# Performance work log

Measured on AMD Instinct MI355X. Metric: run time of the kernel, lower is better.

## Reference

```python
import jax, jax.numpy as jnp
import numpy as np

B, S, H = 4, 512, 256

def setup_inputs() -> dict:
    key = jax.random.key(0)
    k1, k2, k3, k4 = jax.random.split(key, 4)
    scale = 1.0 / np.sqrt(H)
    return {
        "h": jax.random.normal(k1, (B, S, H), dtype=jnp.float32),
        "W_t": jax.random.normal(k2, (H, H), dtype=jnp.float32) * scale,
        "W_t_prime": jax.random.normal(k3, (H, H), dtype=jnp.float32) * scale,
        "b_h": jnp.zeros((H,), dtype=jnp.float32),
        "W_a": jax.random.normal(k4, (H,), dtype=jnp.float32) * scale,
        "b_a": jnp.zeros((), dtype=jnp.float32),
    }

def reference(h, W_t, W_t_prime, b_h, W_a, b_a):
    # Project once per timestep, then broadcast-add over the (t, t') pair grid.
    ht = jnp.einsum("bsh,hk->bsk", h, W_t)          # W_t applied to h^t
    htp = jnp.einsum("bsh,hk->bsk", h, W_t_prime)   # W_{t'} applied to h^{t'}
    # transformed: (B, S_t, S_t', H)
    transformed = ht[:, :, None, :] + htp[:, None, :, :] + b_h
    tanh_out = jnp.tanh(transformed)
    scores = jnp.einsum("bsth,h->bst", tanh_out, W_a) + b_a  # (B, S, S)
    scores = jax.nn.sigmoid(scores)
    attention_weights = jax.nn.softmax(scores, axis=2)
    output = jnp.einsum("bst,bth->bsh", attention_weights, h)
    return output, attention_weights
```

## Files before the change

### kernel.cpp

```cpp
#include <hip/hip_runtime.h>

#define Bn 4
#define Sn 512
#define Hn 256

#define CC   2.8853900817779268f
#define L2E  1.4426950408889634f

typedef __attribute__((ext_vector_type(4))) float f32x4;
typedef __attribute__((ext_vector_type(2))) float f32x2;
typedef __attribute__((ext_vector_type(8))) short short8;

__device__ __forceinline__ unsigned short bf16rn(float f) {
    unsigned int u = __float_as_uint(f);
    u += 0x7fffu + ((u >> 16) & 1u);
    return (unsigned short)(u >> 16);
}
__device__ __forceinline__ float bf16tof(unsigned short b) {
    return __uint_as_float(((unsigned int)b) << 16);
}

__global__ __launch_bounds__(256) void prep_kernel(
    const float* __restrict__ h,  const float* __restrict__ Wt,
    const float* __restrict__ Wp, const float* __restrict__ Wa,
    const float* __restrict__ ba,
    unsigned short* __restrict__ h1, unsigned short* __restrict__ h2,
    unsigned short* __restrict__ wtp,
    float* __restrict__ wa2, float* __restrict__ cst)
{
    __shared__ float tile[64 * 68];
    __shared__ float red4[4];
    const int tid = threadIdx.x;
    const int bid = blockIdx.x;

    if (bid < 256) {
        const int base = (bid * 256 + tid) * 8;
        float4 v0 = *(const float4*)&h[base];
        float4 v1 = *(const float4*)&h[base + 4];
        float f[8] = {v0.x, v0.y, v0.z, v0.w, v1.x, v1.y, v1.z, v1.w};
        unsigned short b1[8], b2[8];
#pragma unroll
        for (int i = 0; i < 8; i++) {
            b1[i] = bf16rn(f[i]);
            b2[i] = bf16rn(f[i] - bf16tof(b1[i]));
        }
        uint4 u1, u2;
        u1.x = (unsigned)b1[0] | ((unsigned)b1[1] << 16);
        u1.y = (unsigned)b1[2] | ((unsigned)b1[3] << 16);
        u1.z = (unsigned)b1[4] | ((unsigned)b1[5] << 16);
        u1.w = (unsigned)b1[6] | ((unsigned)b1[7] << 16);
        u2.x = (unsigned)b2[0] | ((unsigned)b2[1] << 16);
        u2.y = (unsigned)b2[2] | ((unsigned)b2[3] << 16);
        u2.z = (unsigned)b2[4] | ((unsigned)b2[5] << 16);
        u2.w = (unsigned)b2[6] | ((unsigned)b2[7] << 16);
        *(uint4*)&h1[base] = u1;
        *(uint4*)&h2[base] = u2;

        if (bid == 0) {
            float w = Wa[tid];
#pragma unroll
            for (int off = 32; off >= 1; off >>= 1) w += __shfl_xor(w, off, 64);
            if ((tid & 63) == 0) red4[tid >> 6] = w;
            __syncthreads();
            wa2[tid] = -2.0f * Wa[tid];
            if (tid == 0)
                cst[0] = -L2E * ((red4[0] + red4[1] + red4[2] + red4[3]) + ba[0]);
        }
    } else {
        const int sb  = bid - 256;
        const int mat = sb >> 4;
        const int t4  = sb & 15;
        const int k0  = (t4 >> 2) * 64, n0 = (t4 & 3) * 64;
        const float* __restrict__ W = mat ? Wp : Wt;

#pragma unroll
        for (int i = 0; i < 4; i++) {
            const int idx = tid + 256 * i;
            const int kr = idx >> 4, nq = idx & 15;
            *(float4*)&tile[kr * 68 + nq * 4] =
                *(const float4*)&W[(k0 + kr) * Hn + n0 + nq * 4];
        }
        __syncthreads();

        unsigned short* p1 = wtp + mat * 2 * 65536;
        unsigned short* p2 = p1 + 65536;
#pragma unroll
        for (int i = 0; i < 8; i++) {
            const int idx = tid + 256 * i;
            const int n = idx >> 5, kp = idx & 31;
            const float f0 = tile[(2 * kp) * 68 + n];
            const float f1 = tile[(2 * kp + 1) * 68 + n];
            const unsigned short a0 = bf16rn(f0), a1 = bf16rn(f1);
            const unsigned short c0 = bf16rn(f0 - bf16tof(a0));
            const unsigned short c1 = bf16rn(f1 - bf16tof(a1));
            const int dw = ((n0 + n) * 256 + k0) / 2 + kp;
            ((unsigned int*)p1)[dw] = (unsigned)a0 | ((unsigned)a1 << 16);
            ((unsigned int*)p2)[dw] = (unsigned)c0 | ((unsigned)c1 << 16);
        }
    }
}

__global__ __launch_bounds__(256) void gemm_kernel(
    const unsigned short* __restrict__ h1, const unsigned short* __restrict__ h2,
    const unsigned short* __restrict__ wtp, const float* __restrict__ bh,
    float* __restrict__ Egt, float* __restrict__ Egp4)
{
    __shared__ char lds[20480];

    const int tid = threadIdx.x;
    const int mb = blockIdx.x >> 3;
    const int nb = blockIdx.x & 7;
    const int m0 = mb * 64;
    const bool isT = (nb < 4);
    const int n0l = isT ? nb * 64 : (nb - 4) * 64;
    const unsigned short* pB1 = wtp + (isT ? 0 : 2 * 65536);
    const unsigned short* pB2 = pB1 + 65536;

    const int w    = tid >> 6;
    const int lane = tid & 63;
    const int quad = lane >> 4;
    const int l15  = lane & 15;

    f32x4 acc[4];
#pragma unroll
    for (int i = 0; i < 4; i++) acc[i] = (f32x4){0.f, 0.f, 0.f, 0.f};

    const int ssel = tid >> 7;
    const int spl  = (tid >> 6) & 1;
    const int srow = (tid & 63) >> 2;
    const int sseg = tid & 3;
    const unsigned short* gsrc =
        (ssel == 0) ? (spl ? h2 : h1) : (spl ? pB2 : pB1);
    const int growbase = (ssel == 0) ? m0 : n0l;
    char* ldsdst = lds + (ssel * 2 + spl) * 5120;

    for (int ks = 0; ks < 256; ks += 32) {
        __syncthreads();
#pragma unroll
        for (int i = 0; i < 4; i++) {
            const int row = srow + i * 16;
            uint4 v = *(const uint4*)&gsrc[(growbase + row) * 256 + ks + sseg * 8];
            *(uint4*)(ldsdst + row * 80 + sseg * 16) = v;
        }
        __syncthreads();

        const char* Ab = lds;
        const char* Bb = lds + 10240;
        const short8 b1 = *(const short8*)(Bb + (w * 16 + l15) * 80 + quad * 16);
        const short8 b2 = *(const short8*)(Bb + 5120 + (w * 16 + l15) * 80 + quad * 16);
#pragma unroll
        for (int mt = 0; mt < 4; mt++) {
            const short8 a1 = *(const short8*)(Ab + (mt * 16 + l15) * 80 + quad * 16);
            const short8 a2 = *(const short8*)(Ab + 5120 + (mt * 16 + l15) * 80 + quad * 16);
            acc[mt] = __builtin_amdgcn_mfma_f32_16x16x32_bf16(a1, b1, acc[mt], 0, 0, 0);
            acc[mt] = __builtin_amdgcn_mfma_f32_16x16x32_bf16(a1, b2, acc[mt], 0, 0, 0);
            acc[mt] = __builtin_amdgcn_mfma_f32_16x16x32_bf16(a2, b1, acc[mt], 0, 0, 0);
        }
    }

    __syncthreads();
    float* ct = (float*)lds;
#pragma unroll
    for (int mt = 0; mt < 4; mt++)
#pragma unroll
        for (int r = 0; r < 4; r++)
            ct[(mt * 16 + quad * 4 + r) * 68 + w * 16 + l15] = acc[mt][r];
    __syncthreads();

    const int b  = m0 >> 9;
    const int s0 = m0 & 511;
    if (isT) {
        const int n0g = nb * 64;
#pragma unroll
        for (int i = 0; i < 4; i++) {
            const int item = tid + i * 256;
            const int mr = item >> 4, nq = item & 15;
            const float4 c  = *(const float4*)&ct[mr * 68 + nq * 4];
            const float4 bv = *(const float4*)&bh[n0g + nq * 4];
            float4 o;
            o.x = __builtin_amdgcn_exp2f((c.x + bv.x) * CC);
            o.y = __builtin_amdgcn_exp2f((c.y + bv.y) * CC);
            o.z = __builtin_amdgcn_exp2f((c.z + bv.z) * CC);
            o.w = __builtin_amdgcn_exp2f((c.w + bv.w) * CC);
            *(float4*)&Egt[(m0 + mr) * Hn + n0g + nq * 4] = o;
        }
    } else {
        const int kq0 = (nb - 4) * 16;
#pragma unroll
        for (int i = 0; i < 4; i++) {
            const int item = tid + i * 256;
            const int mr = item & 63, nq = item >> 6;
            const float4 c = *(const float4*)&ct[mr * 68 + nq * 4];
            float4 o;
            o.x = __builtin_amdgcn_exp2f(c.x * CC);
            o.y = __builtin_amdgcn_exp2f(c.y * CC);
            o.z = __builtin_amdgcn_exp2f(c.z * CC);
            o.w = __builtin_amdgcn_exp2f(c.w * CC);
            *(float4*)&Egp4[b * 131072 + (kq0 + nq) * 2048 + (s0 + mr) * 4] = o;
        }
    }
}

__global__ __launch_bounds__(512) void attn_kernel(
    const float* __restrict__ hsrc, const float* __restrict__ Egt,
    const float* __restrict__ Egp4, const float* __restrict__ wa2,
    const float* __restrict__ cst,
    float* __restrict__ out, float* __restrict__ out_attn)
{
    __shared__ char smem[26624];
    float*  egt4   = (float*)smem;
    float*  attn_l = (float*)smem;
    float*  wal    = (float*)(smem + 8192);
    float*  red    = (float*)(smem + 9472);
    float4* part   = (float4*)(smem + 10240);

    const int tid = threadIdx.x;
    const int b   = blockIdx.x & 3;
    const int t0  = (blockIdx.x >> 2) << 2;

    for (int i = tid; i < 4 * Hn; i += 512)
        egt4[i] = Egt[(b * Sn + t0) * Hn + i];
    if (tid < 256) wal[tid] = wa2[tid];
    __syncthreads();

    const float4* __restrict__ ep = (const float4*)(Egp4 + b * (Hn * Sn));

    f32x2 accA[4], accB[4];
#pragma unroll
    for (int r = 0; r < 4; r++) { accA[r] = (f32x2){0.f, 0.f}; accB[r] = (f32x2){0.f, 0.f}; }

    float4 cur = ep[tid];
    float4 nxt = ep[Sn + tid];
    for (int k4 = 0; k4 < 64; k4++) {
        const float4 nn = ep[((k4 + 2) & 63) * Sn + tid];
        const float4 w4 = *(const float4*)&wal[k4 * 4];
        const f32x2 wa01 = (f32x2){w4.x, w4.y};
        const f32x2 wa23 = (f32x2){w4.z, w4.w};
        const f32x2 ep01 = (f32x2){cur.x, cur.y};
        const f32x2 ep23 = (f32x2){cur.z, cur.w};
#pragma unroll
        for (int r = 0; r < 4; r++) {
            const float4 eg = *(const float4*)&egt4[r * Hn + k4 * 4];
            const f32x2 d01 = ep01 * (f32x2){eg.x, eg.y} + (f32x2){1.f, 1.f};
            const f32x2 d23 = ep23 * (f32x2){eg.z, eg.w} + (f32x2){1.f, 1.f};
            const float p01 = d01.x * d01.y;
            const float p23 = d23.x * d23.y;
            const float rr  = __builtin_amdgcn_rcpf(p01 * p23);
            const float q23 = p23 * rr;
            const float q01 = p01 * rr;
            const f32x2 m01 = wa01 * (f32x2){d01.y, d01.x};
            const f32x2 m23 = wa23 * (f32x2){d23.y, d23.x};
            accA[r] = accA[r] + m01 * (f32x2){q23, q23};
            accB[r] = accB[r] + m23 * (f32x2){q01, q01};
        }
        cur = nxt; nxt = nn;
    }

    const float k0 = cst[0];
    float ex[4];
#pragma unroll
    for (int r = 0; r < 4; r++) {
        const float a = (accA[r].x + accA[r].y) + (accB[r].x + accB[r].y);
        const float e1  = __builtin_amdgcn_exp2f(fmaf(-L2E, a, k0));
        const float sig = __builtin_amdgcn_rcpf(1.0f + e1);
        ex[r] = __builtin_amdgcn_exp2f(L2E * sig);
    }

    const int lane = tid & 63, wid = tid >> 6;
#pragma unroll
    for (int r = 0; r < 4; r++) {
        float v = ex[r];
#pragma unroll
        for (int off = 32; off >= 1; off >>= 1) v += __shfl_xor(v, off, 64);
        if (lane == 0) red[r * 8 + wid] = v;
    }
    __syncthreads();

#pragma unroll
    for (int r = 0; r < 4; r++) {
        float tot = 0.f;
#pragma unroll
        for (int i = 0; i < 8; i++) tot += red[r * 8 + i];
        const float a = ex[r] * __builtin_amdgcn_rcpf(tot);
        attn_l[r * Sn + tid] = a;
        out_attn[(b * Sn + t0 + r) * Sn + tid] = a;
    }
    __syncthreads();

    const int c4 = tid & 63;
    const int q  = __builtin_amdgcn_readfirstlane(tid >> 6);

    const float* __restrict__ hb = hsrc + (b * Sn + q * 64) * Hn + c4 * 4;

    float4 a[4];
#pragma unroll
    for (int r = 0; r < 4; r++) a[r] = (float4){0.f, 0.f, 0.f, 0.f};

#pragma unroll 2
    for (int j4 = 0; j4 < 16; j4++) {
        float4 wv[4];
#pragma unroll
        for (int r = 0; r < 4; r++)
            wv[r] = *(const float4*)&attn_l[r * Sn + q * 64 + j4 * 4];
#pragma unroll
        for (int i = 0; i < 4; i++) {
            const float4 hv = *(const float4*)&hb[(j4 * 4 + i) * Hn];
#pragma unroll
            for (int r = 0; r < 4; r++) {
                const float wr = ((const float*)&wv[r])[i];
                a[r].x = fmaf(wr, hv.x, a[r].x);
                a[r].y = fmaf(wr, hv.y, a[r].y);
                a[r].z = fmaf(wr, hv.z, a[r].z);
                a[r].w = fmaf(wr, hv.w, a[r].w);
            }
        }
    }
    __syncthreads();

    if (q < 4) {
#pragma unroll
        for (int r = 0; r < 4; r++) part[(q * 4 + r) * 64 + c4] = a[r];
    }
    __syncthreads();
    if (q >= 4) {
#pragma unroll
        for (int r = 0; r < 4; r++) {
            float4 p = part[((q - 4) * 4 + r) * 64 + c4];
            p.x += a[r].x; p.y += a[r].y; p.z += a[r].z; p.w += a[r].w;
            part[((q - 4) * 4 + r) * 64 + c4] = p;
        }
    }
    __syncthreads();

    const int col = tid & 255;
    const int rh  = tid >> 8;
    const float* pf = (const float*)part;
#pragma unroll
    for (int rr = 0; rr < 2; rr++) {
        const int r = rh * 2 + rr;
        float s = 0.f;
#pragma unroll
        for (int qq = 0; qq < 4; qq++)
            s += pf[((qq * 4 + r) * 64 + (col >> 2)) * 4 + (col & 3)];
        out[(b * Sn + t0 + r) * Hn + col] = s;
    }
}

extern "C" void kernel_launch(void* const* d_in, const int* in_sizes, int n_in,
                              void* d_out, int out_size, void* d_ws, size_t ws_size,
                              hipStream_t stream) {
    const float* h   = (const float*)d_in[0];
    const float* Wt  = (const float*)d_in[1];
    const float* Wtp = (const float*)d_in[2];
    const float* bh  = (const float*)d_in[3];
    const float* Wa  = (const float*)d_in[4];
    const float* ba  = (const float*)d_in[5];

    float* out      = (float*)d_out;
    float* out_attn = out + Bn * Sn * Hn;

    float* ws   = (float*)d_ws;
    float* Egt  = ws;
    float* Egp4 = ws + 524288;
    float* wa2  = ws + 1048576;
    float* cst  = ws + 1048832;
    unsigned short* h1  = (unsigned short*)(ws + 1048840);
    unsigned short* h2  = h1 + 2048 * 256;
    unsigned short* wtp = h2 + 2048 * 256;

    prep_kernel<<<dim3(288), dim3(256), 0, stream>>>(
        h, Wt, Wtp, Wa, ba, h1, h2, wtp, wa2, cst);
    gemm_kernel<<<dim3(256), dim3(256), 0, stream>>>(h1, h2, wtp, bh, Egt, Egp4);
    attn_kernel<<<dim3(Bn * (Sn / 4)), dim3(512), 0, stream>>>(
        h, Egt, Egp4, wa2, cst, out, out_attn);
}
```

Before: 124.2 us.

## Split attention hidden-dim reduction across two thread halves with 1024-thread blocks

The attention kernel now launches 1024 threads per block. Each half of the block covers half of the hidden dimension for the score reduction, and the partial sums are combined through shared memory. The per-term math is rewritten as scalar FMAs with one reciprocal per four elements, and the prefetch pipeline is replaced by a plain loop. The output GEMV is also spread over 16 waves instead of 8. This buys more parallelism per block and more latency hiding, at the cost of extra barriers, idle threads during softmax, and possible register pressure under 1024-thread launch bounds.

```diff
diff --git a/kernel.cpp b/kernel.cpp
--- a/kernel.cpp
+++ b/kernel.cpp
@@ -8,7 +8,6 @@
 #define L2E  1.4426950408889634f
 
 typedef __attribute__((ext_vector_type(4))) float f32x4;
-typedef __attribute__((ext_vector_type(2))) float f32x2;
 typedef __attribute__((ext_vector_type(8))) short short8;
 
 __device__ __forceinline__ unsigned short bf16rn(float f) {
@@ -201,146 +200,147 @@
     }
 }
 
-__global__ __launch_bounds__(512) void attn_kernel(
+__global__ __launch_bounds__(1024) void attn_kernel(
     const float* __restrict__ hsrc, const float* __restrict__ Egt,
     const float* __restrict__ Egp4, const float* __restrict__ wa2,
     const float* __restrict__ cst,
     float* __restrict__ out, float* __restrict__ out_attn)
 {
-    __shared__ char smem[26624];
-    float*  egt4   = (float*)smem;
+    __shared__ char smem[40960];
     float*  attn_l = (float*)smem;
-    float*  wal    = (float*)(smem + 8192);
-    float*  red    = (float*)(smem + 9472);
-    float4* part   = (float4*)(smem + 10240);
+    float*  egt4   = (float*)(smem + 8192);
+    float*  wal    = (float*)(smem + 12288);
+    float*  accl   = (float*)(smem + 13312);
+    float*  red    = (float*)(smem + 21504);
+    float4* part   = (float4*)(smem + 8192);
 
     const int tid = threadIdx.x;
+    const int tp  = tid & 511;
+    const int kh  = tid >> 9;
     const int b   = blockIdx.x & 3;
     const int t0  = (blockIdx.x >> 2) << 2;
 
-    for (int i = tid; i < 4 * Hn; i += 512)
-        egt4[i] = Egt[(b * Sn + t0) * Hn + i];
+    egt4[tid & 1023] = Egt[(b * Sn + t0) * Hn + (tid & 1023)];
     if (tid < 256) wal[tid] = wa2[tid];
     __syncthreads();
 
     const float4* __restrict__ ep = (const float4*)(Egp4 + b * (Hn * Sn));
-
-    f32x2 accA[4], accB[4];
-#pragma unroll
-    for (int r = 0; r < 4; r++) { accA[r] = (f32x2){0.f, 0.f}; accB[r] = (f32x2){0.f, 0.f}; }
-
-    float4 cur = ep[tid];
-    float4 nxt = ep[Sn + tid];
-    for (int k4 = 0; k4 < 64; k4++) {
-        const float4 nn = ep[((k4 + 2) & 63) * Sn + tid];
-        const float4 w4 = *(const float4*)&wal[k4 * 4];
-        const f32x2 wa01 = (f32x2){w4.x, w4.y};
-        const f32x2 wa23 = (f32x2){w4.z, w4.w};
-        const f32x2 ep01 = (f32x2){cur.x, cur.y};
-        const f32x2 ep23 = (f32x2){cur.z, cur.w};
+    const int kb = kh * 32;
+
+    float acc[4] = {0.f, 0.f, 0.f, 0.f};
+
+#pragma unroll 2
+    for (int kk = 0; kk < 32; kk++) {
+        const int k4 = kb + kk;
+        const float4 cur = ep[k4 * Sn + tp];
+        const float4 w4  = *(const float4*)&wal[k4 * 4];
 #pragma unroll
         for (int r = 0; r < 4; r++) {
             const float4 eg = *(const float4*)&egt4[r * Hn + k4 * 4];
-            const f32x2 d01 = ep01 * (f32x2){eg.x, eg.y} + (f32x2){1.f, 1.f};
-            const f32x2 d23 = ep23 * (f32x2){eg.z, eg.w} + (f32x2){1.f, 1.f};
-            const float p01 = d01.x * d01.y;
-            const float p23 = d23.x * d23.y;
-            const float rr  = __builtin_amdgcn_rcpf(p01 * p23);
-            const float q23 = p23 * rr;
-            const float q01 = p01 * rr;
-            const f32x2 m01 = wa01 * (f32x2){d01.y, d01.x};
-            const f32x2 m23 = wa23 * (f32x2){d23.y, d23.x};
-            accA[r] = accA[r] + m01 * (f32x2){q23, q23};
-            accB[r] = accB[r] + m23 * (f32x2){q01, q01};
-        }
-        cur = nxt; nxt = nn;
-    }
-
+            const float d1 = fmaf(cur.x, eg.x, 1.0f);
+            const float d2 = fmaf(cur.y, eg.y, 1.0f);
+            const float d3 = fmaf(cur.z, eg.z, 1.0f);
+            const float d4 = fmaf(cur.w, eg.w, 1.0f);
+            const float p12 = d1 * d2, p34 = d3 * d4;
+            const float n12 = fmaf(w4.x, d2, w4.y * d1);
+            const float n34 = fmaf(w4.z, d4, w4.w * d3);
+            const float num = fmaf(n12, p34, n34 * p12);
+            acc[r] = fmaf(num, __builtin_amdgcn_rcpf(p12 * p34), acc[r]);
+        }
+    }
+
+    if (kh == 1) {
+#pragma unroll
+        for (int r = 0; r < 4; r++) accl[r * 512 + tp] = acc[r];
+    }
+    __syncthreads();
+
+    float ex[4];
     const float k0 = cst[0];
-    float ex[4];
-#pragma unroll
-    for (int r = 0; r < 4; r++) {
-        const float a = (accA[r].x + accA[r].y) + (accB[r].x + accB[r].y);
-        const float e1  = __builtin_amdgcn_exp2f(fmaf(-L2E, a, k0));
-        const float sig = __builtin_amdgcn_rcpf(1.0f + e1);
-        ex[r] = __builtin_amdgcn_exp2f(L2E * sig);
-    }
-
-    const int lane = tid & 63, wid = tid >> 6;
-#pragma unroll
-    for (int r = 0; r < 4; r++) {
-        float v = ex[r];
-#pragma unroll
-        for (int off = 32; off >= 1; off >>= 1) v += __shfl_xor(v, off, 64);
-        if (lane == 0) red[r * 8 + wid] = v;
-    }
-    __syncthreads();
-
-#pragma unroll
-    for (int r = 0; r < 4; r++) {
-        float tot = 0.f;
-#pragma unroll
-        for (int i = 0; i < 8; i++) tot += red[r * 8 + i];
-        const float a = ex[r] * __builtin_amdgcn_rcpf(tot);
-        attn_l[r * Sn + tid] = a;
-        out_attn[(b * Sn + t0 + r) * Sn + tid] = a;
+    if (kh == 0) {
+#pragma unroll
+        for (int r = 0; r < 4; r++) {
+            const float a   = acc[r] + accl[r * 512 + tp];
+            const float e1  = __builtin_amdgcn_exp2f(fmaf(-L2E, a, k0));
+            const float sig = __builtin_amdgcn_rcpf(1.0f + e1);
+            ex[r] = __builtin_amdgcn_exp2f(L2E * sig);
+        }
+        const int lane = tid & 63, wid = tid >> 6;
+#pragma unroll
+        for (int r = 0; r < 4; r++) {
+            float v = ex[r];
+#pragma unroll
+            for (int off = 32; off >= 1; off >>= 1) v += __shfl_xor(v, off, 64);
+            if (lane == 0) red[r * 8 + wid] = v;
+        }
+    }
+    __syncthreads();
+
+    if (kh == 0) {
+#pragma unroll
+        for (int r = 0; r < 4; r++) {
+            float tot = 0.f;
+#pragma unroll
+            for (int i = 0; i < 8; i++) tot += red[r * 8 + i];
+            const float a = ex[r] * __builtin_amdgcn_rcpf(tot);
+            attn_l[r * Sn + tp] = a;
+            out_attn[(b * Sn + t0 + r) * Sn + tp] = a;
+        }
     }
     __syncthreads();
 
     const int c4 = tid & 63;
-    const int q  = __builtin_amdgcn_readfirstlane(tid >> 6);
-
-    const float* __restrict__ hb = hsrc + (b * Sn + q * 64) * Hn + c4 * 4;
-
-    float4 a[4];
-#pragma unroll
-    for (int r = 0; r < 4; r++) a[r] = (float4){0.f, 0.f, 0.f, 0.f};
+    const int q  = tid >> 6;
+
+    const float* __restrict__ hb = hsrc + (b * Sn + q * 32) * Hn + c4 * 4;
+
+    float4 a4[4];
+#pragma unroll
+    for (int r = 0; r < 4; r++) a4[r] = (float4){0.f, 0.f, 0.f, 0.f};
 
 #pragma unroll 2
-    for (int j4 = 0; j4 < 16; j4++) {
+    for (int j4 = 0; j4 < 8; j4++) {
         float4 wv[4];
 #pragma unroll
         for (int r = 0; r < 4; r++)
-            wv[r] = *(const float4*)&attn_l[r * Sn + q * 64 + j4 * 4];
+            wv[r] = *(const float4*)&attn_l[r * Sn + q * 32 + j4 * 4];
 #pragma unroll
         for (int i = 0; i < 4; i++) {
             const float4 hv = *(const float4*)&hb[(j4 * 4 + i) * Hn];
 #pragma unroll
             for (int r = 0; r < 4; r++) {
                 const float wr = ((const float*)&wv[r])[i];
-                a[r].x = fmaf(wr, hv.x, a[r].x);
-                a[r].y = fmaf(wr, hv.y, a[r].y);
-                a[r].z = fmaf(wr, hv.z, a[r].z);
-                a[r].w = fmaf(wr, hv.w, a[r].w);
+                a4[r].x = fmaf(wr, hv.x, a4[r].x);
+                a4[r].y = fmaf(wr, hv.y, a4[r].y);
+                a4[r].z = fmaf(wr, hv.z, a4[r].z);
+                a4[r].w = fmaf(wr, hv.w, a4[r].w);
             }
         }
     }
     __syncthreads();
 
-    if (q < 4) {
-#pragma unroll
-        for (int r = 0; r < 4; r++) part[(q * 4 + r) * 64 + c4] = a[r];
-    }
-    __syncthreads();
-    if (q >= 4) {
-#pragma unroll
-        for (int r = 0; r < 4; r++) {
-            float4 p = part[((q - 4) * 4 + r) * 64 + c4];
-            p.x += a[r].x; p.y += a[r].y; p.z += a[r].z; p.w += a[r].w;
-            part[((q - 4) * 4 + r) * 64 + c4] = p;
-        }
-    }
-    __syncthreads();
-
-    const int col = tid & 255;
-    const int rh  = tid >> 8;
-    const float* pf = (const float*)part;
-#pragma unroll
-    for (int rr = 0; rr < 2; rr++) {
-        const int r = rh * 2 + rr;
+    if (q < 8) {
+#pragma unroll
+        for (int r = 0; r < 4; r++) part[(q * 4 + r) * 64 + c4] = a4[r];
+    }
+    __syncthreads();
+    if (q >= 8) {
+#pragma unroll
+        for (int r = 0; r < 4; r++) {
+            float4 p = part[((q - 8) * 4 + r) * 64 + c4];
+            p.x += a4[r].x; p.y += a4[r].y; p.z += a4[r].z; p.w += a4[r].w;
+            part[((q - 8) * 4 + r) * 64 + c4] = p;
+        }
+    }
+    __syncthreads();
+
+    {
+        const int col = tid & 255;
+        const int r   = tid >> 8;
+        const float* pf = (const float*)part;
         float s = 0.f;
 #pragma unroll
-        for (int qq = 0; qq < 4; qq++)
+        for (int qq = 0; qq < 8; qq++)
             s += pf[((qq * 4 + r) * 64 + (col >> 2)) * 4 + (col & 3)];
         out[(b * Sn + t0 + r) * Hn + col] = s;
     }
@@ -371,6 +371,6 @@
     prep_kernel<<<dim3(288), dim3(256), 0, stream>>>(
         h, Wt, Wtp, Wa, ba, h1, h2, wtp, wa2, cst);
     gemm_kernel<<<dim3(256), dim3(256), 0, stream>>>(h1, h2, wtp, bh, Egt, Egp4);
-    attn_kernel<<<dim3(Bn * (Sn / 4)), dim3(512), 0, stream>>>(
+    attn_kernel<<<dim3(Bn * (Sn / 4)), dim3(1024), 0, stream>>>(
         h, Egt, Egp4, wa2, cst, out, out_attn);
 }
```

Result: faster. 118.9 us (-4.3%).
